# Kernel tuning notes

Measured on AMD Instinct MI355X. Metric: run time of the kernel, lower is better.

The kernel has to match this reference:

```python
import jax, jax.numpy as jnp
import numpy as np

N = 100000
E = 1600000
IN, HID, OUT = 128, 128, 64


def gcn_conv(x, W, b, src, dst, n):
    # GCNConv with normalize=True and implicit self-loops:
    # out = D^-1/2 (A+I) D^-1/2 (x W) + b
    ew = jnp.ones(src.shape[0], dtype=x.dtype)  # unit edge weights
    deg = jax.ops.segment_sum(ew, dst, num_segments=n)  # in-degree incl. self-loop
    dinv = jnp.where(deg > 0, jax.lax.rsqrt(deg), 0.0)
    norm = dinv[src] * dinv[dst]  # [E+N]
    h = x @ W  # dense transform first (PyG order)
    msg = h[src] * norm[:, None]  # gather + scale (memory-bound)
    return jax.ops.segment_sum(msg, dst, num_segments=n) + b


def setup_inputs() -> dict:
    key = jax.random.key(0)
    k1, k2, k3, k4, k5, k6 = jax.random.split(key, 6)
    x = jax.random.normal(k1, (N, IN), dtype=jnp.float32)
    edge_index = jax.random.randint(k2, (2, E), 0, N, dtype=jnp.int32)
    s1 = 1.0 / np.sqrt(IN)
    s2 = 1.0 / np.sqrt(HID)
    W1 = jax.random.uniform(k3, (IN, HID), jnp.float32, -s1, s1)
    b1 = jax.random.uniform(k4, (HID,), jnp.float32, -s1, s1)
    W2 = jax.random.uniform(k5, (HID, OUT), jnp.float32, -s2, s2)
    b2 = jax.random.uniform(k6, (OUT,), jnp.float32, -s2, s2)
    return {"x": x, "edge_index": edge_index, "W1": W1, "b1": b1, "W2": W2, "b2": b2}


def reference(x, edge_index, W1, b1, W2, b2):
    n = x.shape[0]
    loops = jnp.arange(n, dtype=edge_index.dtype)
    src = jnp.concatenate([edge_index[0], loops])  # add self-loops
    dst = jnp.concatenate([edge_index[1], loops])
    # eval mode: dropout(p=0.5) is identity
    h = jax.nn.relu(gcn_conv(x, W1, b1, src, dst, n))
    out = gcn_conv(h, W2, b2, src, dst, n)
    return out
```

## Files before the change

kernel.cpp:

```cpp
#include <hip/hip_runtime.h>
#include <hip/hip_fp16.h>
#include <type_traits>

#define NBK 256
#define BSHIFT 9
#define NPB 512
#define BCAP 10240
#define CCAP 12288
#define EPB 4096

template <int N> struct alignas(4 * N) HVec { __half2 v[N]; };

typedef _Float16 half8 __attribute__((ext_vector_type(8)));
typedef float f32x4 __attribute__((ext_vector_type(4)));

__global__ __launch_bounds__(512) void partA_k(const int* __restrict__ src,
                                               const int* __restrict__ dst,
                                               int* __restrict__ cursor,
                                               int* __restrict__ bucketed, int ne) {
    __shared__ int hist[NBK], gbs[NBK], lcur[NBK];
    int t = threadIdx.x;
    int e0 = blockIdx.x * EPB;
    int e1 = min(e0 + EPB, ne);
    for (int i = t; i < NBK; i += 512) { hist[i] = 0; lcur[i] = 0; }
    __syncthreads();
    int sv[EPB / 512], dv[EPB / 512];
#pragma unroll
    for (int k = 0; k < EPB / 512; k++) {
        int e = e0 + t + k * 512;
        int s = 0, d = -1;
        if (e < e1) {
            s = src[e];
            d = dst[e];
            atomicAdd(&hist[d >> BSHIFT], 1);
        }
        sv[k] = s;
        dv[k] = d;
    }
    __syncthreads();
    for (int i = t; i < NBK; i += 512)
        gbs[i] = hist[i] ? atomicAdd(&cursor[i], hist[i]) : 0;
    __syncthreads();
#pragma unroll
    for (int k = 0; k < EPB / 512; k++) {
        if (dv[k] >= 0) {
            int b = dv[k] >> BSHIFT;
            int q = gbs[b] + atomicAdd(&lcur[b], 1);
            if (q < BCAP)
                bucketed[(size_t)b * BCAP + q] = ((dv[k] & (NPB - 1)) << 17) | sv[k];
        }
    }
}

__global__ __launch_bounds__(1024) void csrB_k(const int* __restrict__ bucketed,
                                               const int* __restrict__ cursor,
                                               int* __restrict__ csr,
                                               int* __restrict__ rowbeg,
                                               int* __restrict__ rend,
                                               float* __restrict__ dinv, int nn) {
    __shared__ int cnt[NPB], ofs[NPB], cur[NPB];
    int t = threadIdx.x;
    int b = blockIdx.x;
    int m = min(cursor[b], BCAP);
    const int* bk = bucketed + (size_t)b * BCAP;
    int cbase = b * CCAP;
    if (t < NPB) cnt[t] = 0;
    __syncthreads();
    for (int i = t; i < m; i += 1024)
        atomicAdd(&cnt[bk[i] >> 17], 1);
    __syncthreads();
    int v = 0, pv = 0;
    if (t < NPB) { v = cnt[t]; pv = (v + 3) & ~3; ofs[t] = pv; }
    __syncthreads();
    for (int d = 1; d < NPB; d <<= 1) {
        int u = 0;
        if (t < NPB && t >= d) u = ofs[t - d];
        __syncthreads();
        if (t < NPB) ofs[t] += u;
        __syncthreads();
    }
    if (t < NPB) {
        int ex = ofs[t] - pv;
        cur[t] = ex;
        int node = b * NPB + t;
        if (node < nn) {
            rowbeg[node] = cbase + ex;
            rend[node]   = cbase + ex + pv;
            dinv[node] = rsqrtf((float)(v + 1));
        }
    }
    __syncthreads();
    for (int i = t; i < m; i += 1024) {
        int e = bk[i];
        int p = atomicAdd(&cur[e >> 17], 1);
        csr[cbase + p] = e & 0x1FFFF;
    }
    if (t < NPB) {
        int ex = ofs[t] - pv;
        for (int k = v; k < pv; k++) csr[cbase + ex + k] = nn;
    }
}

__global__ void prepW_k(const float* __restrict__ W1, const float* __restrict__ W2,
                        _Float16* __restrict__ WT1, _Float16* __restrict__ WT2) {
    int i = blockIdx.x * blockDim.x + threadIdx.x;
    if (i < 128 * 128) {
        int k = i >> 7, j = i & 127;
        WT1[j * 128 + k] = (_Float16)W1[i];
    }
    int i2 = i - 128 * 128;
    if (i2 >= 0 && i2 < 128 * 64) {
        int k = i2 >> 6, j = i2 & 63;
        WT2[j * 128 + k] = (_Float16)W2[i2];
    }
}

template <int NO, bool SCALE, typename XT>
__global__ __launch_bounds__(256) void gemm_mfma_k(const XT* __restrict__ X,
                                                   const _Float16* __restrict__ WT,
                                                   const float* __restrict__ dinv,
                                                   _Float16* __restrict__ H, int nrows) {
    constexpr int K = 128;
    constexpr int NCT = NO / 16;
    if (blockIdx.x == 0 && threadIdx.x < NO)
        H[(size_t)nrows * NO + threadIdx.x] = (_Float16)0.f;
    int wv = (int)((blockIdx.x * (size_t)blockDim.x + threadIdx.x) >> 6);
    int r0 = wv * 16;
    if (r0 >= nrows) return;
    int lane = threadIdx.x & 63;
    int lr = lane & 15;
    int kg = lane >> 4;
    int rg = r0 + lr;
    if (rg >= nrows) rg = nrows - 1;

    half8 a[4];
    if constexpr (std::is_same<XT, float>::value) {
#pragma unroll
        for (int ks = 0; ks < 4; ks++) {
            const float* px = X + (size_t)rg * K + ks * 32 + kg * 8;
            float4 x0 = *(const float4*)px;
            float4 x1 = *(const float4*)(px + 4);
            half8 vv;
            vv[0] = (_Float16)x0.x; vv[1] = (_Float16)x0.y;
            vv[2] = (_Float16)x0.z; vv[3] = (_Float16)x0.w;
            vv[4] = (_Float16)x1.x; vv[5] = (_Float16)x1.y;
            vv[6] = (_Float16)x1.z; vv[7] = (_Float16)x1.w;
            a[ks] = vv;
        }
    } else {
#pragma unroll
        for (int ks = 0; ks < 4; ks++)
            a[ks] = *(const half8*)(X + (size_t)rg * K + ks * 32 + kg * 8);
    }

    f32x4 acc[NCT];
#pragma unroll
    for (int ct = 0; ct < NCT; ct++) acc[ct] = (f32x4){0.f, 0.f, 0.f, 0.f};
#pragma unroll
    for (int ct = 0; ct < NCT; ct++) {
#pragma unroll
        for (int ks = 0; ks < 4; ks++) {
            half8 b = *(const half8*)(WT + (size_t)(ct * 16 + lr) * K + ks * 32 + kg * 8);
            acc[ct] = __builtin_amdgcn_mfma_f32_16x16x32_f16(a[ks], b, acc[ct], 0, 0, 0);
        }
    }
#pragma unroll
    for (int i = 0; i < 4; i++) {
        int rr = r0 + kg * 4 + i;
        if (rr < nrows) {
            float s = SCALE ? dinv[rr] : 1.f;
            _Float16* hp = H + (size_t)rr * NO + lr;
#pragma unroll
            for (int ct = 0; ct < NCT; ct++)
                hp[ct * 16] = (_Float16)(acc[ct][i] * s);
        }
    }
}

template <int NF, bool RELU, bool OUTSCALE, typename OutT>
__global__ __launch_bounds__(256) void agg_k(const __half* __restrict__ H,
                                             const int* __restrict__ rowbeg,
                                             const int* __restrict__ rend,
                                             const int* __restrict__ csr,
                                             const float* __restrict__ dinv,
                                             const float* __restrict__ bias,
                                             OutT* __restrict__ Out, int nn) {
    constexpr int VPL = NF / 16;
    constexpr int NV2 = VPL / 2;
    int wid = (int)((blockIdx.x * (size_t)blockDim.x + threadIdx.x) >> 6);
    if (wid >= nn) return;
    int lane = threadIdx.x & 63;
    int g = lane >> 4, t = lane & 15;
    float acc[VPL];
#pragma unroll
    for (int j = 0; j < VPL; j++) acc[j] = 0.f;

    int beg = rowbeg[wid], end = rend[wid];
    int e0 = beg;
    for (; e0 + 16 <= end; e0 += 16) {
        int eb = e0 + g * 4;
        int s0 = csr[eb + 0], s1 = csr[eb + 1], s2 = csr[eb + 2], s3 = csr[eb + 3];
        HVec<NV2> va = *((const HVec<NV2>*)(H + (size_t)s0 * NF) + t);
        HVec<NV2> vb = *((const HVec<NV2>*)(H + (size_t)s1 * NF) + t);
        HVec<NV2> vc = *((const HVec<NV2>*)(H + (size_t)s2 * NF) + t);
        HVec<NV2> vd = *((const HVec<NV2>*)(H + (size_t)s3 * NF) + t);
#pragma unroll
        for (int q = 0; q < NV2; q++) {
            __half2 pab = __hadd2(va.v[q], vb.v[q]);
            __half2 pcd = __hadd2(vc.v[q], vd.v[q]);
            float2 fab = __half22float2(pab);
            float2 fcd = __half22float2(pcd);
            acc[2 * q + 0] += fab.x + fcd.x;
            acc[2 * q + 1] += fab.y + fcd.y;
        }
    }
    for (; e0 < end; e0 += 4) {
        int s = csr[e0 + g];
        HVec<NV2> va = *((const HVec<NV2>*)(H + (size_t)s * NF) + t);
#pragma unroll
        for (int q = 0; q < NV2; q++) {
            float2 f = __half22float2(va.v[q]);
            acc[2 * q + 0] += f.x;
            acc[2 * q + 1] += f.y;
        }
    }
#pragma unroll
    for (int j = 0; j < VPL; j++) {
        acc[j] += __shfl_xor(acc[j], 16);
        acc[j] += __shfl_xor(acc[j], 32);
    }
    HVec<NV2> hn = *((const HVec<NV2>*)(H + (size_t)wid * NF) + t);
#pragma unroll
    for (int q = 0; q < NV2; q++) {
        float2 f = __half22float2(hn.v[q]);
        acc[2 * q + 0] += f.x;
        acc[2 * q + 1] += f.y;
    }
    if (g == 0) {
        float dn = dinv[wid];
        float r[VPL];
#pragma unroll
        for (int j = 0; j < VPL; j++) {
            r[j] = acc[j] * dn + bias[t * VPL + j];
            if (RELU) r[j] = fmaxf(r[j], 0.f);
            if (OUTSCALE) r[j] *= dn;
        }
        if constexpr (std::is_same<OutT, __half>::value) {
            HVec<NV2> o;
#pragma unroll
            for (int q = 0; q < NV2; q++)
                o.v[q] = __floats2half2_rn(r[2 * q], r[2 * q + 1]);
            *((HVec<NV2>*)(Out + (size_t)wid * NF) + t) = o;
        } else {
#pragma unroll
            for (int q = 0; q < VPL / 4; q++) {
                float4 o;
                o.x = r[4 * q + 0]; o.y = r[4 * q + 1];
                o.z = r[4 * q + 2]; o.w = r[4 * q + 3];
                *((float4*)(Out + (size_t)wid * NF) + t * (VPL / 4) + q) = o;
            }
        }
    }
}


extern "C" void kernel_launch(void* const* d_in, const int* in_sizes, int n_in,
                              void* d_out, int out_size, void* d_ws, size_t ws_size,
                              hipStream_t stream) {
    const float* x  = (const float*)d_in[0];
    const int* ei   = (const int*)d_in[1];
    const float* W1 = (const float*)d_in[2];
    const float* b1 = (const float*)d_in[3];
    const float* W2 = (const float*)d_in[4];
    const float* b2 = (const float*)d_in[5];
    float* out = (float*)d_out;

    const int IN = 128, HID = 128;
    int nn = in_sizes[0] / IN;
    int ne = in_sizes[1] / 2;
    const int* src = ei;
    const int* dst = ei + ne;
    int nbuckets = (nn + NPB - 1) / NPB;

    char* w = (char*)d_ws;
    size_t off = 0;
    auto take = [&](size_t bytes) -> void* {
        void* p = w + off;
        off = (off + bytes + 255) & ~(size_t)255;
        return p;
    };
    int*      cursor = (int*)take(NBK * 4);
    int*      rowbeg = (int*)take((size_t)nn * 4);
    int*      rend   = (int*)take((size_t)nn * 4);
    float*    dinv   = (float*)take((size_t)nn * 4);
    int*      csr    = (int*)take((size_t)NBK * CCAP * 4);
    _Float16* WT1    = (_Float16*)take(128 * 128 * 2);
    _Float16* WT2    = (_Float16*)take(64 * 128 * 2);
    _Float16* h      = (_Float16*)take((size_t)(nn + 1) * HID * 2);
    __half*   h1     = (__half*)take((size_t)nn * HID * 2);
    _Float16* h2     = h;
    int*      bucketed = (int*)h;

    (void)ws_size; (void)n_in; (void)out_size;

    hipMemsetAsync(cursor, 0, NBK * 4, stream);

    int tb = 256;
    partA_k<<<(ne + EPB - 1) / EPB, 512, 0, stream>>>(src, dst, cursor, bucketed, ne);
    csrB_k<<<nbuckets, 1024, 0, stream>>>(bucketed, cursor, csr, rowbeg, rend, dinv, nn);
    prepW_k<<<(128 * 128 + 128 * 64 + tb - 1) / tb, tb, 0, stream>>>(W1, W2, WT1, WT2);

    int gblocks = ((nn + 15) / 16 + 3) / 4;

    gemm_mfma_k<128, true, float><<<gblocks, tb, 0, stream>>>(x, WT1, dinv, h, nn);
    agg_k<128, true, true, __half><<<(nn * 64 + tb - 1) / tb, tb, 0, stream>>>(
        (const __half*)h, rowbeg, rend, csr, dinv, b1, h1, nn);

    gemm_mfma_k<64, false, __half><<<gblocks, tb, 0, stream>>>(h1, WT2, dinv, h2, nn);
    agg_k<64, false, false, float><<<(nn * 64 + tb - 1) / tb, tb, 0, stream>>>(
        (const __half*)h2, rowbeg, rend, csr, dinv, b2, out, nn);
}
```

Measured before the change: 205.9 us.

## Specialize 64-wide aggregation with 16-byte lanes, reuse atomic ranks, fuse memset

The second-layer aggregation kernel is rewritten so each lane loads 16 bytes (8 halves) and eight edge groups run per wave, rather than 4-halves-per-lane with four groups. This widens each lane's memory access and gives more gather parallelism per wave. The CSR build now reuses the rank returned by the histogram atomics instead of doing a second atomic pass, and pads rows to a multiple of 8. The cursor memset is folded into the weight-prep kernel, which now runs first. This saves one API call and drops some shared atomics, at the cost of more registers for the stored ranks.

```diff
diff --git a/kernel.cpp b/kernel.cpp
--- a/kernel.cpp
+++ b/kernel.cpp
@@ -14,28 +14,43 @@
 typedef _Float16 half8 __attribute__((ext_vector_type(8)));
 typedef float f32x4 __attribute__((ext_vector_type(4)));
 
+__global__ void prep0_k(const float* __restrict__ W1, const float* __restrict__ W2,
+                        _Float16* __restrict__ WT1, _Float16* __restrict__ WT2,
+                        int* __restrict__ cursor) {
+    int i = blockIdx.x * blockDim.x + threadIdx.x;
+    if (i < NBK) cursor[i] = 0;
+    if (i < 128 * 128) {
+        int k = i >> 7, j = i & 127;
+        WT1[j * 128 + k] = (_Float16)W1[i];
+    }
+    int i2 = i - 128 * 128;
+    if (i2 >= 0 && i2 < 128 * 64) {
+        int k = i2 >> 6, j = i2 & 63;
+        WT2[j * 128 + k] = (_Float16)W2[i2];
+    }
+}
+
 __global__ __launch_bounds__(512) void partA_k(const int* __restrict__ src,
                                                const int* __restrict__ dst,
                                                int* __restrict__ cursor,
                                                int* __restrict__ bucketed, int ne) {
-    __shared__ int hist[NBK], gbs[NBK], lcur[NBK];
+    __shared__ int hist[NBK], gbs[NBK];
     int t = threadIdx.x;
     int e0 = blockIdx.x * EPB;
     int e1 = min(e0 + EPB, ne);
-    for (int i = t; i < NBK; i += 512) { hist[i] = 0; lcur[i] = 0; }
-    __syncthreads();
-    int sv[EPB / 512], dv[EPB / 512];
+    for (int i = t; i < NBK; i += 512) hist[i] = 0;
+    __syncthreads();
+    int sv[EPB / 512], dv[EPB / 512], rv[EPB / 512];
 #pragma unroll
     for (int k = 0; k < EPB / 512; k++) {
         int e = e0 + t + k * 512;
-        int s = 0, d = -1;
+        int s = 0, d = -1, r = 0;
         if (e < e1) {
             s = src[e];
             d = dst[e];
-            atomicAdd(&hist[d >> BSHIFT], 1);
-        }
-        sv[k] = s;
-        dv[k] = d;
+            r = atomicAdd(&hist[d >> BSHIFT], 1);
+        }
+        sv[k] = s; dv[k] = d; rv[k] = r;
     }
     __syncthreads();
     for (int i = t; i < NBK; i += 512)
@@ -45,7 +60,7 @@
     for (int k = 0; k < EPB / 512; k++) {
         if (dv[k] >= 0) {
             int b = dv[k] >> BSHIFT;
-            int q = gbs[b] + atomicAdd(&lcur[b], 1);
+            int q = gbs[b] + rv[k];
             if (q < BCAP)
                 bucketed[(size_t)b * BCAP + q] = ((dv[k] & (NPB - 1)) << 17) | sv[k];
         }
@@ -58,7 +73,7 @@
                                                int* __restrict__ rowbeg,
                                                int* __restrict__ rend,
                                                float* __restrict__ dinv, int nn) {
-    __shared__ int cnt[NPB], ofs[NPB], cur[NPB];
+    __shared__ int cnt[NPB], ofs[NPB], exs[NPB];
     int t = threadIdx.x;
     int b = blockIdx.x;
     int m = min(cursor[b], BCAP);
@@ -66,11 +81,13 @@
     int cbase = b * CCAP;
     if (t < NPB) cnt[t] = 0;
     __syncthreads();
+    int rk[(BCAP + 1023) / 1024];
+    int nit = 0;
     for (int i = t; i < m; i += 1024)
-        atomicAdd(&cnt[bk[i] >> 17], 1);
+        rk[nit++] = atomicAdd(&cnt[bk[i] >> 17], 1);
     __syncthreads();
     int v = 0, pv = 0;
-    if (t < NPB) { v = cnt[t]; pv = (v + 3) & ~3; ofs[t] = pv; }
+    if (t < NPB) { v = cnt[t]; pv = (v + 7) & ~7; ofs[t] = pv; }
     __syncthreads();
     for (int d = 1; d < NPB; d <<= 1) {
         int u = 0;
@@ -81,7 +98,7 @@
     }
     if (t < NPB) {
         int ex = ofs[t] - pv;
-        cur[t] = ex;
+        exs[t] = ex;
         int node = b * NPB + t;
         if (node < nn) {
             rowbeg[node] = cbase + ex;
@@ -90,28 +107,14 @@
         }
     }
     __syncthreads();
+    nit = 0;
     for (int i = t; i < m; i += 1024) {
         int e = bk[i];
-        int p = atomicAdd(&cur[e >> 17], 1);
-        csr[cbase + p] = e & 0x1FFFF;
+        csr[cbase + exs[e >> 17] + rk[nit++]] = e & 0x1FFFF;
     }
     if (t < NPB) {
-        int ex = ofs[t] - pv;
+        int ex = exs[t];
         for (int k = v; k < pv; k++) csr[cbase + ex + k] = nn;
-    }
-}
-
-__global__ void prepW_k(const float* __restrict__ W1, const float* __restrict__ W2,
-                        _Float16* __restrict__ WT1, _Float16* __restrict__ WT2) {
-    int i = blockIdx.x * blockDim.x + threadIdx.x;
-    if (i < 128 * 128) {
-        int k = i >> 7, j = i & 127;
-        WT1[j * 128 + k] = (_Float16)W1[i];
-    }
-    int i2 = i - 128 * 128;
-    if (i2 >= 0 && i2 < 128 * 64) {
-        int k = i2 >> 6, j = i2 & 63;
-        WT2[j * 128 + k] = (_Float16)W2[i2];
     }
 }
 
@@ -177,35 +180,34 @@
     }
 }
 
-template <int NF, bool RELU, bool OUTSCALE, typename OutT>
-__global__ __launch_bounds__(256) void agg_k(const __half* __restrict__ H,
-                                             const int* __restrict__ rowbeg,
-                                             const int* __restrict__ rend,
-                                             const int* __restrict__ csr,
-                                             const float* __restrict__ dinv,
-                                             const float* __restrict__ bias,
-                                             OutT* __restrict__ Out, int nn) {
-    constexpr int VPL = NF / 16;
-    constexpr int NV2 = VPL / 2;
+template <bool RELU, bool OUTSCALE>
+__global__ __launch_bounds__(256) void agg128_k(const __half* __restrict__ H,
+                                                const int* __restrict__ rowbeg,
+                                                const int* __restrict__ rend,
+                                                const int* __restrict__ csr,
+                                                const float* __restrict__ dinv,
+                                                const float* __restrict__ bias,
+                                                __half* __restrict__ Out, int nn) {
+    constexpr int NF = 128;
     int wid = (int)((blockIdx.x * (size_t)blockDim.x + threadIdx.x) >> 6);
     if (wid >= nn) return;
     int lane = threadIdx.x & 63;
     int g = lane >> 4, t = lane & 15;
-    float acc[VPL];
-#pragma unroll
-    for (int j = 0; j < VPL; j++) acc[j] = 0.f;
+    float acc[8];
+#pragma unroll
+    for (int j = 0; j < 8; j++) acc[j] = 0.f;
 
     int beg = rowbeg[wid], end = rend[wid];
     int e0 = beg;
     for (; e0 + 16 <= end; e0 += 16) {
         int eb = e0 + g * 4;
         int s0 = csr[eb + 0], s1 = csr[eb + 1], s2 = csr[eb + 2], s3 = csr[eb + 3];
-        HVec<NV2> va = *((const HVec<NV2>*)(H + (size_t)s0 * NF) + t);
-        HVec<NV2> vb = *((const HVec<NV2>*)(H + (size_t)s1 * NF) + t);
-        HVec<NV2> vc = *((const HVec<NV2>*)(H + (size_t)s2 * NF) + t);
-        HVec<NV2> vd = *((const HVec<NV2>*)(H + (size_t)s3 * NF) + t);
-#pragma unroll
-        for (int q = 0; q < NV2; q++) {
+        HVec<4> va = *((const HVec<4>*)(H + (size_t)s0 * NF) + t);
+        HVec<4> vb = *((const HVec<4>*)(H + (size_t)s1 * NF) + t);
+        HVec<4> vc = *((const HVec<4>*)(H + (size_t)s2 * NF) + t);
+        HVec<4> vd = *((const HVec<4>*)(H + (size_t)s3 * NF) + t);
+#pragma unroll
+        for (int q = 0; q < 4; q++) {
             __half2 pab = __hadd2(va.v[q], vb.v[q]);
             __half2 pcd = __hadd2(vc.v[q], vd.v[q]);
             float2 fab = __half22float2(pab);
@@ -216,50 +218,112 @@
     }
     for (; e0 < end; e0 += 4) {
         int s = csr[e0 + g];
-        HVec<NV2> va = *((const HVec<NV2>*)(H + (size_t)s * NF) + t);
-#pragma unroll
-        for (int q = 0; q < NV2; q++) {
+        HVec<4> va = *((const HVec<4>*)(H + (size_t)s * NF) + t);
+#pragma unroll
+        for (int q = 0; q < 4; q++) {
             float2 f = __half22float2(va.v[q]);
             acc[2 * q + 0] += f.x;
             acc[2 * q + 1] += f.y;
         }
     }
 #pragma unroll
-    for (int j = 0; j < VPL; j++) {
+    for (int j = 0; j < 8; j++) {
         acc[j] += __shfl_xor(acc[j], 16);
         acc[j] += __shfl_xor(acc[j], 32);
     }
-    HVec<NV2> hn = *((const HVec<NV2>*)(H + (size_t)wid * NF) + t);
-#pragma unroll
-    for (int q = 0; q < NV2; q++) {
+    HVec<4> hn = *((const HVec<4>*)(H + (size_t)wid * NF) + t);
+#pragma unroll
+    for (int q = 0; q < 4; q++) {
         float2 f = __half22float2(hn.v[q]);
         acc[2 * q + 0] += f.x;
         acc[2 * q + 1] += f.y;
     }
     if (g == 0) {
         float dn = dinv[wid];
-        float r[VPL];
-#pragma unroll
-        for (int j = 0; j < VPL; j++) {
-            r[j] = acc[j] * dn + bias[t * VPL + j];
+        float r[8];
+#pragma unroll
+        for (int j = 0; j < 8; j++) {
+            r[j] = acc[j] * dn + bias[t * 8 + j];
             if (RELU) r[j] = fmaxf(r[j], 0.f);
             if (OUTSCALE) r[j] *= dn;
         }
-        if constexpr (std::is_same<OutT, __half>::value) {
-            HVec<NV2> o;
-#pragma unroll
-            for (int q = 0; q < NV2; q++)
-                o.v[q] = __floats2half2_rn(r[2 * q], r[2 * q + 1]);
-            *((HVec<NV2>*)(Out + (size_t)wid * NF) + t) = o;
-        } else {
-#pragma unroll
-            for (int q = 0; q < VPL / 4; q++) {
-                float4 o;
-                o.x = r[4 * q + 0]; o.y = r[4 * q + 1];
-                o.z = r[4 * q + 2]; o.w = r[4 * q + 3];
-                *((float4*)(Out + (size_t)wid * NF) + t * (VPL / 4) + q) = o;
-            }
-        }
+        HVec<4> o;
+#pragma unroll
+        for (int q = 0; q < 4; q++)
+            o.v[q] = __floats2half2_rn(r[2 * q], r[2 * q + 1]);
+        *((HVec<4>*)(Out + (size_t)wid * NF) + t) = o;
+    }
+}
+
+template <bool RELU>
+__global__ __launch_bounds__(256) void agg64_k(const __half* __restrict__ H,
+                                               const int* __restrict__ rowbeg,
+                                               const int* __restrict__ rend,
+                                               const int* __restrict__ csr,
+                                               const float* __restrict__ dinv,
+                                               const float* __restrict__ bias,
+                                               float* __restrict__ Out, int nn) {
+    constexpr int NF = 64;
+    int wid = (int)((blockIdx.x * (size_t)blockDim.x + threadIdx.x) >> 6);
+    if (wid >= nn) return;
+    int lane = threadIdx.x & 63;
+    int g = lane >> 3, t = lane & 7;
+    float acc[8];
+#pragma unroll
+    for (int j = 0; j < 8; j++) acc[j] = 0.f;
+
+    int beg = rowbeg[wid], end = rend[wid];
+    int e0 = beg;
+    for (; e0 + 16 <= end; e0 += 16) {
+        int eb = e0 + g * 2;
+        int s0 = csr[eb], s1 = csr[eb + 1];
+        HVec<4> va = *((const HVec<4>*)(H + (size_t)s0 * NF) + t);
+        HVec<4> vb = *((const HVec<4>*)(H + (size_t)s1 * NF) + t);
+#pragma unroll
+        for (int q = 0; q < 4; q++) {
+            __half2 p = __hadd2(va.v[q], vb.v[q]);
+            float2 f = __half22float2(p);
+            acc[2 * q + 0] += f.x;
+            acc[2 * q + 1] += f.y;
+        }
+    }
+    for (; e0 < end; e0 += 8) {
+        int s = csr[e0 + g];
+        HVec<4> va = *((const HVec<4>*)(H + (size_t)s * NF) + t);
+#pragma unroll
+        for (int q = 0; q < 4; q++) {
+            float2 f = __half22float2(va.v[q]);
+            acc[2 * q + 0] += f.x;
+            acc[2 * q + 1] += f.y;
+        }
+    }
+#pragma unroll
+    for (int j = 0; j < 8; j++) {
+        acc[j] += __shfl_xor(acc[j], 8);
+        acc[j] += __shfl_xor(acc[j], 16);
+        acc[j] += __shfl_xor(acc[j], 32);
+    }
+    HVec<4> hn = *((const HVec<4>*)(H + (size_t)wid * NF) + t);
+#pragma unroll
+    for (int q = 0; q < 4; q++) {
+        float2 f = __half22float2(hn.v[q]);
+        acc[2 * q + 0] += f.x;
+        acc[2 * q + 1] += f.y;
+    }
+    if (g == 0) {
+        float dn = dinv[wid];
+        float r[8];
+#pragma unroll
+        for (int j = 0; j < 8; j++) {
+            r[j] = acc[j] * dn + bias[t * 8 + j];
+            if (RELU) r[j] = fmaxf(r[j], 0.f);
+        }
+        float* op = Out + (size_t)wid * NF + t * 8;
+        float4 o0, o1;
+        o0.x = r[0]; o0.y = r[1]; o0.z = r[2]; o0.w = r[3];
+        o1.x = r[4]; o1.y = r[5]; o1.z = r[6]; o1.w = r[7];
+        *(float4*)op = o0;
+        *(float4*)(op + 4) = o1;
     }
 }
 
@@ -303,20 +367,18 @@
 
     (void)ws_size; (void)n_in; (void)out_size;
 
-    hipMemsetAsync(cursor, 0, NBK * 4, stream);
-
     int tb = 256;
+    prep0_k<<<(128 * 128 + 128 * 64 + tb - 1) / tb, tb, 0, stream>>>(W1, W2, WT1, WT2, cursor);
     partA_k<<<(ne + EPB - 1) / EPB, 512, 0, stream>>>(src, dst, cursor, bucketed, ne);
     csrB_k<<<nbuckets, 1024, 0, stream>>>(bucketed, cursor, csr, rowbeg, rend, dinv, nn);
-    prepW_k<<<(128 * 128 + 128 * 64 + tb - 1) / tb, tb, 0, stream>>>(W1, W2, WT1, WT2);
 
     int gblocks = ((nn + 15) / 16 + 3) / 4;
 
     gemm_mfma_k<128, true, float><<<gblocks, tb, 0, stream>>>(x, WT1, dinv, h, nn);
-    agg_k<128, true, true, __half><<<(nn * 64 + tb - 1) / tb, tb, 0, stream>>>(
-        (const __half*)h, rowbeg, rend, csr, dinv, b1, h1, nn);
+    agg128_k<true, true><<<(nn * 64 + tb - 1) / tb, tb, 0, stream>>>(
+        (const __half*)h, rowbeg, rend, csr, dinv, b1, (__half*)h1, nn);
 
     gemm_mfma_k<64, false, __half><<<gblocks, tb, 0, stream>>>(h1, WT2, dinv, h2, nn);
-    agg_k<64, false, false, float><<<(nn * 64 + tb - 1) / tb, tb, 0, stream>>>(
+    agg64_k<false><<<(nn * 64 + tb - 1) / tb, tb, 0, stream>>>(
         (const __half*)h2, rowbeg, rend, csr, dinv, b2, out, nn);
 }
```

After: 202.1 us. About the same (-1.9%).
